# Kernel tuning notes

Measured on AMD Instinct MI355X. Metric: run time of the kernel, lower is better.

Reference implementation:

```python
import jax, jax.numpy as jnp
import numpy as np

N = 20000
E = 640000
F_IN = 128
C_T = 8
L_T = 10 * N
HEADS = 8
HDIM = 64
NEG_SLOPE = 0.2


def setup_inputs() -> dict:
    key = jax.random.key(0)
    ks = jax.random.split(key, 20)
    d = {}
    d["x"] = jax.random.normal(ks[0], (N, F_IN), dtype=jnp.float32)
    d["edge_index"] = jax.random.randint(ks[1], (2, E), 0, N, dtype=jnp.int64)
    d["temporal"] = jax.random.normal(ks[2], (C_T, L_T), dtype=jnp.float32)
    # GCNConv(F_IN, 16)
    d["W1"] = jax.random.normal(ks[3], (F_IN, 16), dtype=jnp.float32) * 0.1
    d["b1"] = jnp.zeros((16,), dtype=jnp.float32)
    # GATConv(16, 64, heads=8), concat -> 512
    d["W2"] = jax.random.normal(ks[4], (16, HEADS * HDIM), dtype=jnp.float32) * 0.1
    d["att_src"] = jax.random.normal(ks[5], (HEADS, HDIM), dtype=jnp.float32) * 0.1
    d["att_dst"] = jax.random.normal(ks[6], (HEADS, HDIM), dtype=jnp.float32) * 0.1
    d["b2"] = jnp.zeros((HEADS * HDIM,), dtype=jnp.float32)
    # TemporalCNN
    d["cw1"] = jax.random.normal(ks[7], (32, C_T, 3), dtype=jnp.float32) * 0.1
    d["cb1"] = jnp.zeros((32,), dtype=jnp.float32)
    d["cw2"] = jax.random.normal(ks[8], (64, 32, 3), dtype=jnp.float32) * 0.05
    d["cb2"] = jnp.zeros((64,), dtype=jnp.float32)
    d["cw3"] = jax.random.normal(ks[9], (128, 64, 3), dtype=jnp.float32) * 0.05
    d["cb3"] = jnp.zeros((128,), dtype=jnp.float32)
    d["fw1"] = jax.random.normal(ks[10], (256, 128 * 10), dtype=jnp.float32) * 0.02
    d["fb1"] = jnp.zeros((256,), dtype=jnp.float32)
    d["fw2"] = jax.random.normal(ks[11], (64, 256), dtype=jnp.float32) * 0.05
    d["fb2"] = jnp.zeros((64,), dtype=jnp.float32)
    return d


def _conv1d(x, w, b):
    # x: [1, C, L], w: [O, C, 3]; padding=1 == SAME for k=3
    out = jax.lax.conv_general_dilated(
        x, w, window_strides=(1,), padding="SAME",
        dimension_numbers=("NCH", "OIH", "NCH"))
    return out + b[None, :, None]


def _gcn(x, src, dst, W, b):
    # PyG GCNConv: add self-loops, symmetric normalization
    h = x @ W                                   # [N, 16]
    deg = jax.ops.segment_sum(jnp.ones_like(dst, dtype=h.dtype), dst, num_segments=N)
    dinv = jax.lax.rsqrt(jnp.maximum(deg, 1.0))
    norm = dinv[src] * dinv[dst]                # [E+N]
    out = jax.ops.segment_sum(h[src] * norm[:, None], dst, num_segments=N)
    return out + b


def _gat(x, src, dst, W, att_src, att_dst, b):
    h = (x @ W).reshape(N, HEADS, HDIM)         # [N, 8, 64]
    a_s = jnp.einsum("nhd,hd->nh", h, att_src)  # [N, 8]
    a_d = jnp.einsum("nhd,hd->nh", h, att_dst)
    e = a_s[src] + a_d[dst]                     # [E+N, 8], message j->i: src=j, dst=i
    e = jnp.where(e >= 0, e, NEG_SLOPE * e)     # LeakyReLU(0.2)
    # segment softmax over incoming edges of each dst node
    m = jax.ops.segment_max(e, dst, num_segments=N)
    m = jnp.where(jnp.isfinite(m), m, 0.0)
    ex = jnp.exp(e - m[dst])
    s = jax.ops.segment_sum(ex, dst, num_segments=N)
    alpha = ex / (s[dst] + 1e-16)               # [E+N, 8]
    out = jax.ops.segment_sum(h[src] * alpha[:, :, None], dst, num_segments=N)
    return out.reshape(N, HEADS * HDIM) + b


def reference(x, edge_index, temporal, W1, b1, W2, att_src, att_dst, b2,
              cw1, cb1, cw2, cb2, cw3, cb3, fw1, fb1, fw2, fb2):
    # ---- graph branch ----
    loops = jnp.arange(N, dtype=edge_index.dtype)
    src = jnp.concatenate([edge_index[0], loops])
    dst = jnp.concatenate([edge_index[1], loops])
    g = _gcn(x, src, dst, W1, b1)
    g = jax.nn.relu(g)
    # F.dropout with training=False (eval) -> identity
    x1 = _gat(g, src, dst, W2, att_src, att_dst, b2)   # [N, 512]
    # ---- temporal branch ----
    t = temporal[None]                                  # [1, C, L]
    t = jax.nn.relu(_conv1d(t, cw1, cb1))
    t = jax.nn.relu(_conv1d(t, cw2, cb2))
    t = jax.nn.relu(_conv1d(t, cw3, cb3))               # [1, 128, L]
    t = t.reshape(-1, 128 * 10)                         # [N, 1280] (same as torch .view)
    t = jax.nn.relu(t @ fw1.T + fb1)
    x2 = t @ fw2.T + fb2                                # [N, 64]
    return jnp.concatenate([x1, x2], axis=1)            # [N, 576]
```

## Files before the change

### kernel.cpp

```cpp
#include <hip/hip_runtime.h>
#include <hip/hip_bf16.h>

#define NN 20000
#define EE 640000
#define FIN 128
#define CT 8
#define LT 200000
#define HEADS 8
#define HDIM 64
#define F1 16
#define F2 512
#define OUTF 576

typedef short s16x8 __attribute__((ext_vector_type(8)));
typedef float f32x4 __attribute__((ext_vector_type(4)));

static __device__ __forceinline__ float b2f(__hip_bfloat16 v) { return __bfloat162float(v); }
static __device__ __forceinline__ float ldf(float v) { return v; }
static __device__ __forceinline__ float ldf(__hip_bfloat16 v) { return __bfloat162float(v); }
static __device__ __forceinline__ unsigned f2bf_bits(float x) {
  unsigned u = __float_as_uint(x);
  return (u + 0x7fffu + ((u >> 16) & 1u)) >> 16;
}

static __device__ __forceinline__ void gl16(const void* g, void* l) {
  __builtin_amdgcn_global_load_lds(
      (const __attribute__((address_space(1))) unsigned*)g,
      (__attribute__((address_space(3))) unsigned*)l, 16, 0, 0);
}


__global__ __launch_bounds__(256) void wprep_kernel(
    const float* __restrict__ cw, float* __restrict__ wt, int O, int C) {
  int i = blockIdx.x * 256 + threadIdx.x;
  if (i >= O * C * 3) return;
  int o = i / (C * 3), r = i % (C * 3);
  int c = r / 3, k = r % 3;
  wt[(c * 3 + k) * O + o] = cw[i];
}

__global__ __launch_bounds__(256) void wprep_bf(
    const float* __restrict__ cw, short* __restrict__ wb, int O, int C) {
  int i = blockIdx.x * 256 + threadIdx.x;
  if (i >= O * C * 3) return;
  int o = i / (C * 3), r = i % (C * 3);
  int ic = r / 3, kk = r % 3;
  wb[o * 3 * C + kk * C + ic] = (short)f2bf_bits(cw[i]);
}

template <int C, int O, int P, typename IN_T>
__global__ __launch_bounds__(256) void conv_fast(
    const IN_T* __restrict__ in, __hip_bfloat16* __restrict__ out,
    const float* __restrict__ wt, const float* __restrict__ bias) {
  constexpr int OCG = O / 2;
  constexpr int PG = 256 / OCG;
  static_assert(PG * P == 64, "tile mismatch");
  __shared__ __align__(16) float tile[C][68];
  __shared__ __align__(16) __hip_bfloat16 ot[O][66];
  int t = threadIdx.x;
  int ocg = t % OCG;
  int pg = t / OCG;
  long base = (long)blockIdx.x * 64;

  for (int i = t; i < C * 66; i += 256) {
    int c = i / 66, p = i % 66;
    long l = base + p - 1;
    tile[c][p] = (l >= 0 && l < LT) ? ldf(in[(long)c * LT + l]) : 0.f;
  }
  __syncthreads();

  int oc0 = 2 * ocg;
  int p0 = pg * P;
  float acc[2][P];
#pragma unroll
  for (int j = 0; j < 2; j++)
#pragma unroll
    for (int p = 0; p < P; p++) acc[j][p] = 0.f;

  for (int ic = 0; ic < C; ic++) {
    float x[P + 2];
#pragma unroll
    for (int q = 0; q < P / 4; q++) {
      float4 v = *(const float4*)&tile[ic][p0 + 4 * q];
      x[4 * q] = v.x; x[4 * q + 1] = v.y; x[4 * q + 2] = v.z; x[4 * q + 3] = v.w;
    }
    {
      float2 v = *(const float2*)&tile[ic][p0 + P];
      x[P] = v.x; x[P + 1] = v.y;
    }
    const float* wrow = wt + (long)ic * 3 * O;
    float wv[3][2];
#pragma unroll
    for (int kk = 0; kk < 3; kk++) {
      float2 w2 = *(const float2*)&wrow[kk * O + oc0];
      wv[kk][0] = w2.x; wv[kk][1] = w2.y;
    }
#pragma unroll
    for (int kk = 0; kk < 3; kk++)
#pragma unroll
      for (int j = 0; j < 2; j++)
#pragma unroll
        for (int p = 0; p < P; p++) acc[j][p] += x[p + kk] * wv[kk][j];
  }
  float b0 = bias[oc0], b1 = bias[oc0 + 1];
#pragma unroll
  for (int p = 0; p < P; p++) {
    ot[oc0][p0 + p] = __float2bfloat16(fmaxf(acc[0][p] + b0, 0.f));
    ot[oc0 + 1][p0 + p] = __float2bfloat16(fmaxf(acc[1][p] + b1, 0.f));
  }
  __syncthreads();
  for (int i = t; i < O * 32; i += 256) {
    int oc = i >> 5, pp = i & 31;
    unsigned v = ((const unsigned*)&ot[oc][0])[pp];
    *(unsigned*)&out[(long)oc * LT + base + 2 * pp] = v;
  }
}

template <int C, int O, int MPW>
__global__ __launch_bounds__(256) void conv_mfma(
    const short* __restrict__ in, short* __restrict__ out,
    const short* __restrict__ w, const float* __restrict__ bias) {
  constexpr int K = 3 * C;
  constexpr int NS = K / 32;
  constexpr int XP = C + 8;
  constexpr int OP = 132;
  constexpr int SH_X = 132 * XP * 2;
  constexpr int SH_O = O * OP * 2;
  __shared__ __align__(16) char smem[(SH_X > SH_O) ? SH_X : SH_O];
  short* xT = (short*)smem;

  int t = threadIdx.x;
  long base = (long)blockIdx.x * 128;

  for (int idx = t; idx < C * 132; idx += 256) {
    int ic = idx / 132, p = idx % 132;
    long l = base + p - 1;
    xT[p * XP + ic] = (l >= 0 && l < LT) ? in[(long)ic * LT + l] : (short)0;
  }
  __syncthreads();

  int wave = t >> 6, lane = t & 63;
  int n = lane & 15, kg = lane >> 4;
  int m0 = wave * (MPW * 16);

  f32x4 acc[MPW][8] = {};
#pragma unroll
  for (int s = 0; s < NS; s++) {
    const int kk = (s * 32) / C;
    const int ic0 = (s * 32) % C + kg * 8;
    s16x8 a[MPW];
#pragma unroll
    for (int mi = 0; mi < MPW; mi++)
      a[mi] = *(const s16x8*)(w + (long)(m0 + mi * 16 + n) * K + s * 32 + kg * 8);
#pragma unroll
    for (int nt = 0; nt < 8; nt++) {
      s16x8 b = *(const s16x8*)(xT + (nt * 16 + n + kk) * XP + ic0);
#pragma unroll
      for (int mi = 0; mi < MPW; mi++)
        acc[mi][nt] = __builtin_amdgcn_mfma_f32_16x16x32_bf16(a[mi], b, acc[mi][nt], 0, 0, 0);
    }
  }

  __syncthreads();
  short* ob = (short*)smem;
#pragma unroll
  for (int mi = 0; mi < MPW; mi++) {
    int o = m0 + mi * 16 + kg * 4;
#pragma unroll
    for (int nt = 0; nt < 8; nt++) {
      int p = nt * 16 + n;
#pragma unroll
      for (int r = 0; r < 4; r++) {
        float v = fmaxf(acc[mi][nt][r] + bias[o + r], 0.f);
        ob[(o + r) * OP + p] = (short)f2bf_bits(v);
      }
    }
  }
  __syncthreads();
  const unsigned* obu = (const unsigned*)smem;
  for (int idx = t; idx < O * 64; idx += 256) {
    int o = idx >> 6, q = idx & 63;
    long l = base + 2 * q;
    if (l < LT)
      *(unsigned*)(out + (long)o * LT + l) = obu[o * (OP / 2) + q];
  }
}

__global__ __launch_bounds__(256) void fw1bf_kernel(
    const float* __restrict__ fw1, __hip_bfloat16* __restrict__ w) {
  int i = blockIdx.x * 256 + threadIdx.x;
  if (i < 256 * 1280) w[i] = __float2bfloat16(fw1[i]);
}

__global__ __launch_bounds__(256) void fw2t_kernel(
    const float* __restrict__ fw2, float* __restrict__ fw2t) {
  int i = blockIdx.x * 256 + threadIdx.x;
  if (i >= 64 * 256) return;
  int o = i / 256, j = i % 256;
  fw2t[j * 64 + o] = fw2[i];
}

__global__ __launch_bounds__(256) void fc1_tile(
    const __hip_bfloat16* __restrict__ t3, const __hip_bfloat16* __restrict__ w,
    const float* __restrict__ fb1, float* __restrict__ out) {
  __shared__ __align__(16) short As[2][128 * 32];
  __shared__ __align__(16) short Bs[2][128 * 32];
  int t = threadIdx.x;
  int wid = t >> 6, lane = t & 63;
  int bn = blockIdx.x & 1, bm = blockIdx.x >> 1;
  int mrow = lane & 15, kg = lane >> 4;

  const char* tb = (const char*)t3;
  const char* wb = (const char*)w;
  int u0 = wid * 128 + lane;
  int u1 = u0 + 64;
  int ra0 = u0 >> 2, ca0 = u0 & 3;
  int ra1 = u1 >> 2, ca1 = u1 & 3;
  long ga0 = ((long)min(bm * 128 + ra0, NN - 1) * 1280 + ca0 * 8) * 2;
  long ga1 = ((long)min(bm * 128 + ra1, NN - 1) * 1280 + ca1 * 8) * 2;
  long gb0 = ((long)(bn * 128 + ra0) * 1280 + ca0 * 8) * 2;
  long gb1 = ((long)(bn * 128 + ra1) * 1280 + ca1 * 8) * 2;
  int l0 = (wid * 2 + 0) * 512;
  int l1 = (wid * 2 + 1) * 512;

#define FC1_STAGE(buf, k0)                          \
  do {                                              \
    long kb = (long)(k0) * 2;                       \
    gl16(tb + ga0 + kb, &As[buf][l0]);              \
    gl16(tb + ga1 + kb, &As[buf][l1]);              \
    gl16(wb + gb0 + kb, &Bs[buf][l0]);              \
    gl16(wb + gb1 + kb, &Bs[buf][l1]);              \
  } while (0)

  FC1_STAGE(0, 0);
  __syncthreads();

  int wr = wid >> 1, wc = wid & 1;
  f32x4 acc[4][4] = {};
  for (int s = 0; s < 40; s++) {
    int buf = s & 1;
    if (s + 1 < 40) FC1_STAGE(buf ^ 1, (s + 1) * 32);
    s16x8 a[4], b[4];
#pragma unroll
    for (int mi = 0; mi < 4; mi++)
      a[mi] = *(const s16x8*)&As[buf][(wr * 64 + mi * 16 + mrow) * 32 + kg * 8];
#pragma unroll
    for (int ni = 0; ni < 4; ni++)
      b[ni] = *(const s16x8*)&Bs[buf][(wc * 64 + ni * 16 + mrow) * 32 + kg * 8];
#pragma unroll
    for (int mi = 0; mi < 4; mi++)
#pragma unroll
      for (int ni = 0; ni < 4; ni++)
        acc[mi][ni] = __builtin_amdgcn_mfma_f32_16x16x32_bf16(a[mi], b[ni], acc[mi][ni], 0, 0, 0);
    __syncthreads();
  }
#undef FC1_STAGE

  int node_base = bm * 128 + wr * 64 + kg * 4;
  int col_base = bn * 128 + wc * 64 + mrow;
#pragma unroll
  for (int ni = 0; ni < 4; ni++) {
    int col = col_base + ni * 16;
    float bias = fb1[col];
#pragma unroll
    for (int mi = 0; mi < 4; mi++) {
      int node = node_base + mi * 16;
#pragma unroll
      for (int r = 0; r < 4; r++) {
        if (node + r < NN)
          out[(long)(node + r) * 256 + col] = fmaxf(acc[mi][ni][r] + bias, 0.f);
      }
    }
  }
}

__global__ __launch_bounds__(256) void fc2_kernel(
    const float* __restrict__ fc1o, const float* __restrict__ fw2t,
    const float* __restrict__ fb2, float* __restrict__ out) {
  __shared__ float sh[32][257];
  int t = threadIdx.x;
  int m0 = blockIdx.x * 32;
  for (int i = t; i < 32 * 256; i += 256) {
    int nd = i >> 8, j = i & 255;
    sh[nd][j] = fc1o[(long)(m0 + nd) * 256 + j];
  }
  __syncthreads();
  int wave = t >> 6, o = t & 63;
  int nb = wave * 8;
  float acc[8];
  float bias = fb2[o];
#pragma unroll
  for (int i = 0; i < 8; i++) acc[i] = bias;
  for (int j = 0; j < 256; j++) {
    float wv = fw2t[j * 64 + o];
#pragma unroll
    for (int i = 0; i < 8; i++) acc[i] += sh[nb + i][j] * wv;
  }
#pragma unroll
  for (int i = 0; i < 8; i++)
    out[(long)(m0 + nb + i) * OUTF + F2 + o] = acc[i];
}


__global__ __launch_bounds__(256) void zero_i32(int* __restrict__ p, int n) {
  int i = blockIdx.x * 256 + threadIdx.x;
  if (i < n) p[i] = 0;
}

__global__ __launch_bounds__(256) void deg_kernel(const int* __restrict__ dst, int* __restrict__ deg) {
  int e = blockIdx.x * 256 + threadIdx.x;
  if (e < EE) atomicAdd(&deg[dst[e]], 1);
}

__global__ __launch_bounds__(256) void dinv_kernel(const int* __restrict__ deg, float* __restrict__ dinv) {
  int i = blockIdx.x * 256 + threadIdx.x;
  if (i < NN) dinv[i] = rsqrtf((float)(deg[i] + 1));
}

__global__ __launch_bounds__(1024) void scan_kernel(const int* __restrict__ deg, int* __restrict__ offs) {
  __shared__ int sums[1024];
  int tid = threadIdx.x;
  const int CH = 20;
  int s = 0;
  for (int i = 0; i < CH; i++) {
    int idx = tid * CH + i;
    if (idx < NN) s += deg[idx] + 1;
  }
  sums[tid] = s;
  __syncthreads();
  for (int off = 1; off < 1024; off <<= 1) {
    int v = (tid >= off) ? sums[tid - off] : 0;
    __syncthreads();
    sums[tid] += v;
    __syncthreads();
  }
  int run = (tid > 0) ? sums[tid - 1] : 0;
  for (int i = 0; i < CH; i++) {
    int idx = tid * CH + i;
    if (idx < NN) {
      offs[idx] = run;
      run += deg[idx] + 1;
    }
  }
  if (tid == 1023) offs[NN] = sums[1023];
}

__global__ __launch_bounds__(256) void fill_kernel(
    const int* __restrict__ src, const int* __restrict__ dst,
    const int* __restrict__ offs, int* __restrict__ cursor, int* __restrict__ csr) {
  int e = blockIdx.x * 256 + threadIdx.x;
  if (e < EE) {
    int d = dst[e];
    int pos = atomicAdd(&cursor[d], 1);
    csr[offs[d] + pos] = src[e];
  } else if (e < EE + NN) {
    int i = e - EE;
    int pos = atomicAdd(&cursor[i], 1);
    csr[offs[i] + pos] = i;
  }
}

__global__ __launch_bounds__(256) void h1_kernel(
    const float* __restrict__ x, const float* __restrict__ W1,
    float* __restrict__ h1) {
  int idx = blockIdx.x * 256 + threadIdx.x;
  if (idx >= NN * F1) return;
  int n = idx >> 4, f = idx & 15;
  float acc = 0.f;
  for (int k = 0; k < FIN; k++) acc += x[n * FIN + k] * W1[k * F1 + f];
  h1[idx] = acc;
}

__global__ __launch_bounds__(64) void gcn_kernel(
    const float* __restrict__ h1, const int* __restrict__ offs, const int* __restrict__ csr,
    const float* __restrict__ dinv, const float* __restrict__ b1, float* __restrict__ g) {
  int i = blockIdx.x;
  int tid = threadIdx.x;
  int f = tid & 15, grp = tid >> 4;
  int beg = offs[i], end = offs[i + 1];
  float acc = 0.f;
  for (int idx = beg + grp; idx < end; idx += 4) {
    int s = csr[idx];
    acc += h1[s * F1 + f] * dinv[s];
  }
  acc += __shfl_down(acc, 32);
  acc += __shfl_down(acc, 16);
  if (tid < 16) g[i * F1 + f] = fmaxf(acc * dinv[i] + b1[f], 0.f);
}

__global__ __launch_bounds__(256) void att_prep(
    const float* __restrict__ W2, const float* __restrict__ asrc,
    const float* __restrict__ adst, float* __restrict__ WS, float* __restrict__ WD) {
  int t = threadIdx.x;
  int k = (t & 127) >> 3, h = t & 7;
  const float* av = (t < 128) ? asrc : adst;
  float acc = 0.f;
  for (int d = 0; d < 64; d++) acc += W2[k * F2 + h * 64 + d] * av[h * 64 + d];
  ((t < 128) ? WS : WD)[k * 8 + h] = acc;
}

__global__ __launch_bounds__(256) void h2att_kernel(
    const float* __restrict__ g, const float* __restrict__ W2,
    const float* __restrict__ WS, const float* __restrict__ WD,
    unsigned* __restrict__ h2hm, float* __restrict__ AS, float* __restrict__ AD) {
  __shared__ __align__(16) float gl[32][20];
  int t = threadIdx.x;
  int i0 = blockIdx.x * 32;
  for (int idx = t; idx < 512; idx += 256)
    gl[idx >> 4][idx & 15] = g[i0 * 16 + idx];
  __syncthreads();

  int f0 = 2 * t;
  int h = t >> 5, c32 = t & 31;
  float w0[16], w1[16];
#pragma unroll
  for (int k = 0; k < 16; k++) {
    float2 wv = *(const float2*)&W2[k * F2 + f0];
    w0[k] = wv.x; w1[k] = wv.y;
  }
  for (int nl = 0; nl < 32; nl++) {
    float a0 = 0.f, a1 = 0.f;
#pragma unroll
    for (int kk = 0; kk < 4; kk++) {
      f32x4 gv = *(const f32x4*)&gl[nl][4 * kk];
#pragma unroll
      for (int r = 0; r < 4; r++) {
        a0 += gv[r] * w0[4 * kk + r];
        a1 += gv[r] * w1[4 * kk + r];
      }
    }
    h2hm[((long)h * NN + i0 + nl) * 32 + c32] = f2bf_bits(a0) | (f2bf_bits(a1) << 16);
  }
  int nl = t >> 3, hh = t & 7;
  float s = 0.f, d = 0.f;
#pragma unroll
  for (int k = 0; k < 16; k++) {
    float gv = gl[nl][k];
    s += gv * WS[k * 8 + hh];
    d += gv * WD[k * 8 + hh];
  }
  AS[(long)hh * NN + i0 + nl] = s;
  AD[(long)hh * NN + i0 + nl] = d;
}

__global__ __launch_bounds__(256) void gat_fused_kernel(
    const unsigned* __restrict__ h2hm, const float* __restrict__ AS,
    const float* __restrict__ AD, const int* __restrict__ offs,
    const int* __restrict__ csr, const float* __restrict__ b2,
    float* __restrict__ out) {
  __shared__ __align__(16) unsigned long long pairs[4][64];
  __shared__ __align__(16) float accb[4][8][68];
  int h = blockIdx.x & 7;
  int gn = blockIdx.x >> 3;
  int wave = threadIdx.x >> 6;
  int lane = threadIdx.x & 63;
  int i = gn * 4 + wave;
  int beg = offs[i], end = offs[i + 1];
  const float* ASh = AS + (long)h * NN;
  float ad = AD[(long)h * NN + i];
  const char* hb2 = (const char*)(h2hm + (long)h * NN * 32);
  int octet = lane >> 3, q = lane & 7;
  unsigned laneoff = (unsigned)q * 16u;
  unsigned long long* prs = &pairs[wave][0];

  float acc[8] = {0.f, 0.f, 0.f, 0.f, 0.f, 0.f, 0.f, 0.f};
  float sum = 0.f;

  for (int c = beg; c < end; c += 64) {
    int cnt = end - c;
    if (cnt > 64) cnt = 64;
    unsigned off = 0u;
    float ex = 0.f;
    if (lane < cnt) {
      int s = csr[c + lane];
      float e = ASh[s] + ad;
      e = (e >= 0.f) ? e : 0.2f * e;
      ex = __expf(e);
      sum += ex;
      off = (unsigned)s << 7;
    }
    asm volatile("" ::: "memory");
    prs[lane] = ((unsigned long long)__float_as_uint(ex) << 32) | off;
    asm volatile("" ::: "memory");
    int nj = (cnt + 7) >> 3;
    const unsigned long long* pp = prs + octet;
#pragma unroll 2
    for (int j = 0; j < nj; j++) {
      unsigned long long pr = pp[(long)j * 8];
      unsigned voff = (unsigned)pr | laneoff;
      float aj = __uint_as_float((unsigned)(pr >> 32));
      uint4 v = *(const uint4*)(hb2 + voff);
      acc[0] += __uint_as_float(v.x << 16) * aj;
      acc[1] += __uint_as_float(v.x & 0xffff0000u) * aj;
      acc[2] += __uint_as_float(v.y << 16) * aj;
      acc[3] += __uint_as_float(v.y & 0xffff0000u) * aj;
      acc[4] += __uint_as_float(v.z << 16) * aj;
      acc[5] += __uint_as_float(v.z & 0xffff0000u) * aj;
      acc[6] += __uint_as_float(v.w << 16) * aj;
      acc[7] += __uint_as_float(v.w & 0xffff0000u) * aj;
    }
    asm volatile("" ::: "memory");
  }
#pragma unroll
  for (int o = 32; o > 0; o >>= 1) sum += __shfl_xor(sum, o, 64);
  float rinv = 1.f / (sum + 1e-16f);
  float* ab = &accb[wave][octet][q * 8];
  f32x4 lo = {acc[0], acc[1], acc[2], acc[3]};
  f32x4 hi = {acc[4], acc[5], acc[6], acc[7]};
  *(f32x4*)ab = lo;
  *(f32x4*)(ab + 4) = hi;
  asm volatile("" ::: "memory");
  float r = 0.f;
#pragma unroll
  for (int o = 0; o < 8; o++) r += accb[wave][o][lane];
  out[(long)i * OUTF + h * 64 + lane] = r * rinv + b2[h * 64 + lane];
}


extern "C" void kernel_launch(void* const* d_in, const int* in_sizes, int n_in,
                              void* d_out, int out_size, void* d_ws, size_t ws_size,
                              hipStream_t stream) {
  const float* x        = (const float*)d_in[0];
  const int*   eidx     = (const int*)d_in[1];
  const float* temporal = (const float*)d_in[2];
  const float* W1       = (const float*)d_in[3];
  const float* b1       = (const float*)d_in[4];
  const float* W2       = (const float*)d_in[5];
  const float* att_src  = (const float*)d_in[6];
  const float* att_dst  = (const float*)d_in[7];
  const float* b2       = (const float*)d_in[8];
  const float* cw1      = (const float*)d_in[9];
  const float* cb1      = (const float*)d_in[10];
  const float* cw2      = (const float*)d_in[11];
  const float* cb2      = (const float*)d_in[12];
  const float* cw3      = (const float*)d_in[13];
  const float* cb3      = (const float*)d_in[14];
  const float* fw1      = (const float*)d_in[15];
  const float* fb1      = (const float*)d_in[16];
  const float* fw2      = (const float*)d_in[17];
  const float* fb2      = (const float*)d_in[18];
  float* out = (float*)d_out;

  const int* e_src = eidx;
  const int* e_dst = eidx + EE;

  char* ws = (char*)d_ws;
  __hip_bfloat16* T1b = (__hip_bfloat16*)(ws + 0);
  __hip_bfloat16* T2b = (__hip_bfloat16*)(ws + 12800000);
  __hip_bfloat16* T3b = (__hip_bfloat16*)(ws + 38400000);
  __hip_bfloat16* FW1BF = (__hip_bfloat16*)(ws + 0);
  float* FW2T   = (float*)(ws + 655360);
  float* FC1OUT = (float*)(ws + 1310720);
  float* H1     = (float*)(ws + 0);
  float* G      = (float*)(ws + 1280000);
  int*   DEG    = (int*)  (ws + 2560000);
  float* DINV   = (float*)(ws + 2640000);
  int*   OFFS   = (int*)  (ws + 2720000);
  int*   CURSOR = (int*)  (ws + 2800128);
  int*   CSR    = (int*)  (ws + 2880128);
  float* AS     = (float*)(ws + 5520128);
  float* AD     = (float*)(ws + 6160128);
  unsigned* H2HM = (unsigned*)(ws + 6800128);
  float* WSM    = (float*)(ws + 2560000);
  float* WDM    = (float*)(ws + 2560512);
  float* WT1 = out;
  short* WB2 = (short*)((char*)d_out + 3072);
  short* WB3 = (short*)((char*)d_out + 15360);

  const int PB = LT / 64;
  const int MB = (LT + 127) / 128;

  wprep_kernel<<<(32 * 8 * 3 + 255) / 256, 256, 0, stream>>>(cw1, WT1, 32, 8);
  wprep_bf<<<(64 * 32 * 3 + 255) / 256, 256, 0, stream>>>(cw2, WB2, 64, 32);
  wprep_bf<<<(128 * 64 * 3 + 255) / 256, 256, 0, stream>>>(cw3, WB3, 128, 64);
  conv_fast<8, 32, 4, float><<<PB, 256, 0, stream>>>(temporal, T1b, WT1, cb1);
  conv_mfma<32, 64, 1><<<MB, 256, 0, stream>>>((const short*)T1b, (short*)T2b, WB2, cb2);
  fw1bf_kernel<<<(256 * 1280 + 255) / 256, 256, 0, stream>>>(fw1, FW1BF);
  fw2t_kernel<<<(64 * 256 + 255) / 256, 256, 0, stream>>>(fw2, FW2T);
  conv_mfma<64, 128, 2><<<MB, 256, 0, stream>>>((const short*)T2b, (short*)T3b, WB3, cb3);
  fc1_tile<<<157 * 2, 256, 0, stream>>>(T3b, FW1BF, fb1, FC1OUT);
  fc2_kernel<<<NN / 32, 256, 0, stream>>>(FC1OUT, FW2T, fb2, out);

  zero_i32<<<(NN + 255) / 256, 256, 0, stream>>>(DEG, NN);
  zero_i32<<<(NN + 255) / 256, 256, 0, stream>>>(CURSOR, NN);
  deg_kernel<<<(EE + 255) / 256, 256, 0, stream>>>(e_dst, DEG);
  dinv_kernel<<<(NN + 255) / 256, 256, 0, stream>>>(DEG, DINV);
  scan_kernel<<<1, 1024, 0, stream>>>(DEG, OFFS);
  att_prep<<<1, 256, 0, stream>>>(W2, att_src, att_dst, WSM, WDM);
  fill_kernel<<<(EE + NN + 255) / 256, 256, 0, stream>>>(e_src, e_dst, OFFS, CURSOR, CSR);
  h1_kernel<<<(NN * F1 + 255) / 256, 256, 0, stream>>>(x, W1, H1);
  gcn_kernel<<<NN, 64, 0, stream>>>(H1, OFFS, CSR, DINV, b1, G);
  h2att_kernel<<<NN / 32, 256, 0, stream>>>(G, W2, WSM, WDM, H2HM, AS, AD);
  gat_fused_kernel<<<(NN / 4) * 8, 256, 0, stream>>>(H2HM, AS, AD, OFFS, CSR, b2, out);
}
```

Before: 475.2 us.

## Tile h1 GEMM in LDS, prescale by dinv, pack GAT FMAs, merge zero launches

The h1 projection now stages the x rows and W1 in shared memory, and it multiplies by dinv[src] when writing, so the GCN gather no longer loads dinv per edge. The GCN kernel packs 4 nodes per 256-thread block instead of one node per 64-thread block. The GAT inner loop is manually unrolled by two with f32x2 accumulators, intended to let the compiler emit packed FMAs. The two zeroing launches become one over a range that is assumed to hold DEG and CURSOR contiguously, which depends on the workspace layout.

```diff
diff --git a/kernel.cpp b/kernel.cpp
--- a/kernel.cpp
+++ b/kernel.cpp
@@ -14,6 +14,7 @@
 
 typedef short s16x8 __attribute__((ext_vector_type(8)));
 typedef float f32x4 __attribute__((ext_vector_type(4)));
+typedef float f32x2 __attribute__((ext_vector_type(2)));
 
 static __device__ __forceinline__ float b2f(__hip_bfloat16 v) { return __bfloat162float(v); }
 static __device__ __forceinline__ float ldf(float v) { return v; }
@@ -362,30 +363,42 @@
 
 __global__ __launch_bounds__(256) void h1_kernel(
     const float* __restrict__ x, const float* __restrict__ W1,
-    float* __restrict__ h1) {
-  int idx = blockIdx.x * 256 + threadIdx.x;
-  if (idx >= NN * F1) return;
-  int n = idx >> 4, f = idx & 15;
+    const float* __restrict__ dinv, float* __restrict__ h1s) {
+  __shared__ __align__(16) float ws[128 * 16];
+  __shared__ __align__(16) float xs[16][132];
+  int t = threadIdx.x;
+  int i0 = blockIdx.x * 16;
+#pragma unroll
+  for (int i = t; i < 512; i += 256)
+    *(float4*)&ws[4 * i] = *(const float4*)&W1[4 * i];
+#pragma unroll
+  for (int i = t; i < 512; i += 256) {
+    int nl = i >> 5, q = i & 31;
+    *(float4*)&xs[nl][4 * q] = *(const float4*)&x[(long)(i0 + nl) * FIN + 4 * q];
+  }
+  __syncthreads();
+  int nl = t >> 4, f = t & 15;
   float acc = 0.f;
-  for (int k = 0; k < FIN; k++) acc += x[n * FIN + k] * W1[k * F1 + f];
-  h1[idx] = acc;
-}
-
-__global__ __launch_bounds__(64) void gcn_kernel(
-    const float* __restrict__ h1, const int* __restrict__ offs, const int* __restrict__ csr,
+#pragma unroll 8
+  for (int k = 0; k < FIN; k++) acc += xs[nl][k] * ws[k * 16 + f];
+  int n = i0 + nl;
+  h1s[n * F1 + f] = acc * dinv[n];
+}
+
+__global__ __launch_bounds__(256) void gcn_kernel(
+    const float* __restrict__ h1s, const int* __restrict__ offs, const int* __restrict__ csr,
     const float* __restrict__ dinv, const float* __restrict__ b1, float* __restrict__ g) {
-  int i = blockIdx.x;
-  int tid = threadIdx.x;
-  int f = tid & 15, grp = tid >> 4;
+  int wave = threadIdx.x >> 6;
+  int lane = threadIdx.x & 63;
+  int i = blockIdx.x * 4 + wave;
+  int f = lane & 15, grp = lane >> 4;
   int beg = offs[i], end = offs[i + 1];
   float acc = 0.f;
-  for (int idx = beg + grp; idx < end; idx += 4) {
-    int s = csr[idx];
-    acc += h1[s * F1 + f] * dinv[s];
-  }
+  for (int idx = beg + grp; idx < end; idx += 4)
+    acc += h1s[csr[idx] * F1 + f];
   acc += __shfl_down(acc, 32);
   acc += __shfl_down(acc, 16);
-  if (tid < 16) g[i * F1 + f] = fmaxf(acc * dinv[i] + b1[f], 0.f);
+  if (lane < 16) g[i * F1 + f] = fmaxf(acc * dinv[i] + b1[f], 0.f);
 }
 
 __global__ __launch_bounds__(256) void att_prep(
@@ -441,6 +454,18 @@
   }
   AS[(long)hh * NN + i0 + nl] = s;
   AD[(long)hh * NN + i0 + nl] = d;
+}
+
+static __device__ __forceinline__ void acc8(f32x2* a, uint4 v, float aj) {
+  f32x2 aj2 = {aj, aj};
+  f32x2 t0 = {__uint_as_float(v.x << 16), __uint_as_float(v.x & 0xffff0000u)};
+  f32x2 t1 = {__uint_as_float(v.y << 16), __uint_as_float(v.y & 0xffff0000u)};
+  f32x2 t2 = {__uint_as_float(v.z << 16), __uint_as_float(v.z & 0xffff0000u)};
+  f32x2 t3 = {__uint_as_float(v.w << 16), __uint_as_float(v.w & 0xffff0000u)};
+  a[0] += t0 * aj2;
+  a[1] += t1 * aj2;
+  a[2] += t2 * aj2;
+  a[3] += t3 * aj2;
 }
 
 __global__ __launch_bounds__(256) void gat_fused_kernel(
@@ -463,7 +488,7 @@
   unsigned laneoff = (unsigned)q * 16u;
   unsigned long long* prs = &pairs[wave][0];
 
-  float acc[8] = {0.f, 0.f, 0.f, 0.f, 0.f, 0.f, 0.f, 0.f};
+  f32x2 acc2[4] = {};
   float sum = 0.f;
 
   for (int c = beg; c < end; c += 64) {
@@ -484,20 +509,19 @@
     asm volatile("" ::: "memory");
     int nj = (cnt + 7) >> 3;
     const unsigned long long* pp = prs + octet;
-#pragma unroll 2
-    for (int j = 0; j < nj; j++) {
+    int j = 0;
+    for (; j + 2 <= nj; j += 2) {
+      unsigned long long pr0 = pp[(long)j * 8];
+      unsigned long long pr1 = pp[(long)j * 8 + 8];
+      uint4 v0 = *(const uint4*)(hb2 + ((unsigned)pr0 | laneoff));
+      uint4 v1 = *(const uint4*)(hb2 + ((unsigned)pr1 | laneoff));
+      acc8(acc2, v0, __uint_as_float((unsigned)(pr0 >> 32)));
+      acc8(acc2, v1, __uint_as_float((unsigned)(pr1 >> 32)));
+    }
+    if (j < nj) {
       unsigned long long pr = pp[(long)j * 8];
-      unsigned voff = (unsigned)pr | laneoff;
-      float aj = __uint_as_float((unsigned)(pr >> 32));
-      uint4 v = *(const uint4*)(hb2 + voff);
-      acc[0] += __uint_as_float(v.x << 16) * aj;
-      acc[1] += __uint_as_float(v.x & 0xffff0000u) * aj;
-      acc[2] += __uint_as_float(v.y << 16) * aj;
-      acc[3] += __uint_as_float(v.y & 0xffff0000u) * aj;
-      acc[4] += __uint_as_float(v.z << 16) * aj;
-      acc[5] += __uint_as_float(v.z & 0xffff0000u) * aj;
-      acc[6] += __uint_as_float(v.w << 16) * aj;
-      acc[7] += __uint_as_float(v.w & 0xffff0000u) * aj;
+      uint4 v = *(const uint4*)(hb2 + ((unsigned)pr | laneoff));
+      acc8(acc2, v, __uint_as_float((unsigned)(pr >> 32)));
     }
     asm volatile("" ::: "memory");
   }
@@ -505,8 +529,8 @@
   for (int o = 32; o > 0; o >>= 1) sum += __shfl_xor(sum, o, 64);
   float rinv = 1.f / (sum + 1e-16f);
   float* ab = &accb[wave][octet][q * 8];
-  f32x4 lo = {acc[0], acc[1], acc[2], acc[3]};
-  f32x4 hi = {acc[4], acc[5], acc[6], acc[7]};
+  f32x4 lo = {acc2[0][0], acc2[0][1], acc2[1][0], acc2[1][1]};
+  f32x4 hi = {acc2[2][0], acc2[2][1], acc2[3][0], acc2[3][1]};
   *(f32x4*)ab = lo;
   *(f32x4*)(ab + 4) = hi;
   asm volatile("" ::: "memory");
@@ -581,15 +605,14 @@
   fc1_tile<<<157 * 2, 256, 0, stream>>>(T3b, FW1BF, fb1, FC1OUT);
   fc2_kernel<<<NN / 32, 256, 0, stream>>>(FC1OUT, FW2T, fb2, out);
 
-  zero_i32<<<(NN + 255) / 256, 256, 0, stream>>>(DEG, NN);
-  zero_i32<<<(NN + 255) / 256, 256, 0, stream>>>(CURSOR, NN);
+  zero_i32<<<(80032 + 255) / 256, 256, 0, stream>>>(DEG, 80032);
   deg_kernel<<<(EE + 255) / 256, 256, 0, stream>>>(e_dst, DEG);
   dinv_kernel<<<(NN + 255) / 256, 256, 0, stream>>>(DEG, DINV);
   scan_kernel<<<1, 1024, 0, stream>>>(DEG, OFFS);
   att_prep<<<1, 256, 0, stream>>>(W2, att_src, att_dst, WSM, WDM);
   fill_kernel<<<(EE + NN + 255) / 256, 256, 0, stream>>>(e_src, e_dst, OFFS, CURSOR, CSR);
-  h1_kernel<<<(NN * F1 + 255) / 256, 256, 0, stream>>>(x, W1, H1);
-  gcn_kernel<<<NN, 64, 0, stream>>>(H1, OFFS, CSR, DINV, b1, G);
+  h1_kernel<<<NN / 16, 256, 0, stream>>>(x, W1, DINV, H1);
+  gcn_kernel<<<NN / 4, 256, 0, stream>>>(H1, OFFS, CSR, DINV, b1, G);
   h2att_kernel<<<NN / 32, 256, 0, stream>>>(G, W2, WSM, WDM, H2HM, AS, AD);
   gat_fused_kernel<<<(NN / 4) * 8, 256, 0, stream>>>(H2HM, AS, AD, OFFS, CSR, b2, out);
 }
```

After: 467.6 us. No clear change (-1.6%).
